# Optimization experiments

Measured on AMD Instinct MI355X. Metric: run time of the kernel, lower is better.

The kernel has to match this reference:

```python
import jax, jax.numpy as jnp
import numpy as np
from jax.scipy.special import gammaln

N_I = 100000
N_J = 100000
D = 8
S_I = 6000
S_J = 6000
NNZ = 500000
EPS = 1e-06


def setup_inputs() -> dict:
    key = jax.random.key(0)
    ks = jax.random.split(key, 9)
    beta = jax.random.normal(ks[0], (N_I,), dtype=jnp.float32)
    gamma = jax.random.normal(ks[1], (N_J,), dtype=jnp.float32)
    latent_zi = jax.random.normal(ks[2], (N_I, D), dtype=jnp.float32)
    latent_zj = jax.random.normal(ks[3], (N_J, D), dtype=jnp.float32)
    # multinomial-without-replacement node samples -> random permutation prefix
    sample_i_idx = jax.random.permutation(ks[4], N_I)[:S_I]
    sample_j_idx = jax.random.permutation(ks[5], N_J)[:S_J]
    # spspmm-selected subgraph links (global node indices) with edge counts
    sparse_i_sample = jax.random.randint(ks[6], (NNZ,), 0, N_I)
    sparse_j_sample = jax.random.randint(ks[7], (NNZ,), 0, N_J)
    valueC = jax.random.uniform(ks[8], (NNZ,), dtype=jnp.float32)
    return {
        'beta': beta, 'gamma': gamma,
        'latent_zi': latent_zi, 'latent_zj': latent_zj,
        'valueC': valueC,
        'sample_i_idx': sample_i_idx, 'sample_j_idx': sample_j_idx,
        'sparse_i_sample': sparse_i_sample, 'sparse_j_sample': sparse_j_sample,
    }


def reference(beta, gamma, latent_zi, latent_zj, valueC,
              sample_i_idx, sample_j_idx, sparse_i_sample, sparse_j_sample):
    # Dense non-link term over sampled (I, J) block
    zi = latent_zi[sample_i_idx]            # [S_I, D]
    zj = latent_zj[sample_j_idx]            # [S_J, D]
    diff = zi[:, None, :] - zj[None, :, :] + EPS   # [S_I, S_J, D]
    z_dist = jnp.sqrt(jnp.sum(diff * diff, axis=-1))  # [S_I, S_J]
    Lambda = beta[sample_i_idx][:, None] + gamma[sample_j_idx][None, :] - z_dist
    # Sparse link terms (Poisson log-likelihood)
    dl = latent_zi[sparse_i_sample] - latent_zj[sparse_j_sample] + EPS  # [NNZ, D]
    z_dist_links = jnp.sqrt(jnp.sum(dl * dl, axis=-1))                  # [NNZ]
    bias_links = beta[sparse_i_sample] + gamma[sparse_j_sample]
    log_Lambda_links = valueC * (bias_links - z_dist_links)
    LL = jnp.sum(log_Lambda_links - gammaln(valueC + 1.0)) - jnp.sum(jnp.exp(Lambda))
    return LL
```

## Files before the change

kernel.cpp:

```cpp
#include <hip/hip_runtime.h>
#include <hip/hip_fp16.h>
#include <math.h>

#define NI_TOT 100000
#define NJ_TOT 100000
#define DD 8
#define SI_N 6000
#define SJ_N 6000
#define NNZ_N 500000
#define EPSF 1e-6f
#define LOG2E 1.44269504088896f

#define TI 64
#define JPT 2
#define JTILE (256 * JPT)
#define ND_I ((SI_N + TI - 1) / TI)
#define NJT ((SJ_N + JTILE - 1) / JTILE)
#define N_DENSE_BLOCKS (ND_I * NJT)
#define LPT 4
#define SPARSE_SPAN (256 * LPT)
#define N_SPARSE_BLOCKS ((NNZ_N + SPARSE_SPAN - 1) / SPARSE_SPAN)
#define N_TOTAL_BLOCKS (N_DENSE_BLOCKS + N_SPARSE_BLOCKS)

#define NROWS (NI_TOT + NJ_TOT)
#define HZ_BYTES ((size_t)NROWS * DD * 2)
#define HB_BYTES ((size_t)NROWS * 2)

#define GA1 (-0.577191652f)
#define GA2 ( 0.988205891f)
#define GA3 (-0.897056937f)
#define GA4 ( 0.918206857f)
#define GA5 (-0.756704078f)
#define GA6 ( 0.482199394f)
#define GA7 (-0.193527818f)
#define GA8 ( 0.035868343f)

__global__ __launch_bounds__(256) void pack_kernel(
    const float* __restrict__ beta, const float* __restrict__ gamma,
    const float* __restrict__ zi_all, const float* __restrict__ zj_all,
    __half* __restrict__ hz, __half* __restrict__ hb)
{
    const int r = blockIdx.x * 256 + threadIdx.x;
    if (r < NROWS) {
        const float* src = (r < NI_TOT) ? zi_all + (size_t)r * DD
                                        : zj_all + (size_t)(r - NI_TOT) * DD;
        float4 a = ((const float4*)src)[0];
        float4 b = ((const float4*)src)[1];
        __half2 h0 = __floats2half2_rn(a.x, a.y);
        __half2 h1 = __floats2half2_rn(a.z, a.w);
        __half2 h2 = __floats2half2_rn(b.x, b.y);
        __half2 h3 = __floats2half2_rn(b.z, b.w);
        uint4 u;
        u.x = *(unsigned*)&h0; u.y = *(unsigned*)&h1;
        u.z = *(unsigned*)&h2; u.w = *(unsigned*)&h3;
        ((uint4*)hz)[r] = u;
    } else if (r < 2 * NROWS) {
        const int q = r - NROWS;
        float v = (q < NI_TOT) ? beta[q] : gamma[q - NI_TOT];
        hb[q] = __float2half(v);
    }
}

__device__ __forceinline__ void unpack_row(uint4 u, float f[DD]) {
    float2 p;
    p = __half22float2(*(__half2*)&u.x); f[0] = p.x; f[1] = p.y;
    p = __half22float2(*(__half2*)&u.y); f[2] = p.x; f[3] = p.y;
    p = __half22float2(*(__half2*)&u.z); f[4] = p.x; f[5] = p.y;
    p = __half22float2(*(__half2*)&u.w); f[6] = p.x; f[7] = p.y;
}

__global__ __launch_bounds__(256) void fused_kernel(
    const float* __restrict__ beta, const float* __restrict__ gamma,
    const float* __restrict__ zi_all, const float* __restrict__ zj_all,
    const float* __restrict__ valueC,
    const int* __restrict__ si, const int* __restrict__ sj,
    const int* __restrict__ spi, const int* __restrict__ spj,
    const __half* __restrict__ hz, const __half* __restrict__ hb,
    float* __restrict__ out, int mode)
{
    __shared__ float sRed[4];
    const int t = threadIdx.x;

    float blocksum = 0.0f;

    if (blockIdx.x < N_DENSE_BLOCKS) {
        __shared__ __align__(16) float  sZi[TI * DD];
        __shared__ __align__(8)  float2 sIB[TI];

        const int it = blockIdx.x % ND_I;
        const int js = blockIdx.x / ND_I;
        const int i0 = it * TI;

        for (int idx = t; idx < TI * DD; idx += 256) {
            int r = idx >> 3, d = idx & 7;
            int gi = i0 + r;
            float v = (gi < SI_N) ? zi_all[(size_t)si[gi] * DD + d] : 0.0f;
            sZi[idx] = (v + EPSF) * LOG2E;
        }
        __syncthreads();
        if (t < TI) {
            int gi = i0 + t;
            float s = 0.0f;
#pragma unroll
            for (int d = 0; d < DD; ++d) {
                float v = sZi[t * DD + d];
                s = fmaf(v, v, s);
            }
            float bL = (gi < SI_N) ? beta[si[gi]] * LOG2E : -1e30f;
            sIB[t] = make_float2(s, bL);
        }

        const int jb = js * JTILE + t * JPT;
        float zA[DD], zB[DD], glA, glB, s2A, s2B;
        {
            int gj = jb;
            if (gj < SJ_N) {
                int row = sj[gj];
                const float4* q = (const float4*)(zj_all + (size_t)row * DD);
                float4 q0 = q[0], q1 = q[1];
                zA[0]=q0.x*LOG2E; zA[1]=q0.y*LOG2E; zA[2]=q0.z*LOG2E; zA[3]=q0.w*LOG2E;
                zA[4]=q1.x*LOG2E; zA[5]=q1.y*LOG2E; zA[6]=q1.z*LOG2E; zA[7]=q1.w*LOG2E;
                glA = gamma[row] * LOG2E;
            } else {
#pragma unroll
                for (int d = 0; d < DD; ++d) zA[d] = 0.0f;
                glA = -1e30f;
            }
            gj = jb + 1;
            if (gj < SJ_N) {
                int row = sj[gj];
                const float4* q = (const float4*)(zj_all + (size_t)row * DD);
                float4 q0 = q[0], q1 = q[1];
                zB[0]=q0.x*LOG2E; zB[1]=q0.y*LOG2E; zB[2]=q0.z*LOG2E; zB[3]=q0.w*LOG2E;
                zB[4]=q1.x*LOG2E; zB[5]=q1.y*LOG2E; zB[6]=q1.z*LOG2E; zB[7]=q1.w*LOG2E;
                glB = gamma[row] * LOG2E;
            } else {
#pragma unroll
                for (int d = 0; d < DD; ++d) zB[d] = 0.0f;
                glB = -1e30f;
            }
            float sa = 0.0f, sb = 0.0f;
#pragma unroll
            for (int d = 0; d < DD; ++d) {
                sa = fmaf(zA[d], zA[d], sa);
                sb = fmaf(zB[d], zB[d], sb);
            }
            s2A = sa; s2B = sb;
        }
        __syncthreads();

        float acc0 = 0.0f, acc1 = 0.0f;
        float4 cr0 = *(const float4*)&sZi[0];
        float4 cr1 = *(const float4*)&sZi[4];
        float2 cib = sIB[0];
#pragma unroll 4
        for (int a = 0; a < TI; ++a) {
            float4 nr0, nr1; float2 nib;
            if (a + 1 < TI) {
                nr0 = *(const float4*)&sZi[(a + 1) * DD];
                nr1 = *(const float4*)&sZi[(a + 1) * DD + 4];
                nib = sIB[a + 1];
            }
            float dA = 0.0f, dB = 0.0f;
            dA = fmaf(cr0.x, zA[0], dA); dB = fmaf(cr0.x, zB[0], dB);
            dA = fmaf(cr0.y, zA[1], dA); dB = fmaf(cr0.y, zB[1], dB);
            dA = fmaf(cr0.z, zA[2], dA); dB = fmaf(cr0.z, zB[2], dB);
            dA = fmaf(cr0.w, zA[3], dA); dB = fmaf(cr0.w, zB[3], dB);
            dA = fmaf(cr1.x, zA[4], dA); dB = fmaf(cr1.x, zB[4], dB);
            dA = fmaf(cr1.y, zA[5], dA); dB = fmaf(cr1.y, zB[5], dB);
            dA = fmaf(cr1.z, zA[6], dA); dB = fmaf(cr1.z, zB[6], dB);
            dA = fmaf(cr1.w, zA[7], dA); dB = fmaf(cr1.w, zB[7], dB);
            float ssA = fmaf(dA, -2.0f, cib.x + s2A);
            float ssB = fmaf(dB, -2.0f, cib.x + s2B);
            ssA = fmaxf(ssA, 1e-20f);
            ssB = fmaxf(ssB, 1e-20f);
            float xA = cib.y + glA - __builtin_amdgcn_sqrtf(ssA);
            float xB = cib.y + glB - __builtin_amdgcn_sqrtf(ssB);
            acc0 += __builtin_amdgcn_exp2f(xA);
            acc1 += __builtin_amdgcn_exp2f(xB);
            cr0 = nr0; cr1 = nr1; cib = nib;
        }
        blocksum = -(acc0 + acc1);
    } else {
        const int base = (blockIdx.x - N_DENSE_BLOCKS) * SPARSE_SPAN + t;
        float val = 0.0f;
        const uint4* hzv = (const uint4*)hz;
#pragma unroll
        for (int u = 0; u < LPT; ++u) {
            const int idx = base + u * 256;
            if (idx >= NNZ_N) continue;
            const int i = spi[idx], j = spj[idx];
            const float c = valueC[idx];
            float dist, bg;
            if (mode == 0) {
                uint4 ui = hzv[i];
                uint4 uj = hzv[NI_TOT + j];
                float fi[DD], fj[DD];
                unpack_row(ui, fi);
                unpack_row(uj, fj);
                float ss = 0.0f;
#pragma unroll
                for (int d = 0; d < DD; ++d) {
                    float df = fi[d] - fj[d] + EPSF;
                    ss = fmaf(df, df, ss);
                }
                ss = fmaxf(ss, 1e-20f);
                dist = __builtin_amdgcn_sqrtf(ss);
                bg = __half2float(hb[i]) + __half2float(hb[NI_TOT + j]);
            } else {
                const float4* zi4 = (const float4*)(zi_all + (size_t)i * DD);
                const float4* zj4 = (const float4*)(zj_all + (size_t)j * DD);
                float4 a0 = zi4[0], a1 = zi4[1];
                float4 b0 = zj4[0], b1 = zj4[1];
                float ss = 0.0f, df;
                df = a0.x-b0.x+EPSF; ss = fmaf(df,df,ss);
                df = a0.y-b0.y+EPSF; ss = fmaf(df,df,ss);
                df = a0.z-b0.z+EPSF; ss = fmaf(df,df,ss);
                df = a0.w-b0.w+EPSF; ss = fmaf(df,df,ss);
                df = a1.x-b1.x+EPSF; ss = fmaf(df,df,ss);
                df = a1.y-b1.y+EPSF; ss = fmaf(df,df,ss);
                df = a1.z-b1.z+EPSF; ss = fmaf(df,df,ss);
                df = a1.w-b1.w+EPSF; ss = fmaf(df,df,ss);
                ss = fmaxf(ss, 1e-20f);
                dist = __builtin_amdgcn_sqrtf(ss);
                bg = beta[i] + gamma[j];
            }
            float g = 1.0f + c*(GA1 + c*(GA2 + c*(GA3 + c*(GA4 + c*(GA5
                          + c*(GA6 + c*(GA7 + c*GA8)))))));
            val += c * (bg - dist) - __builtin_amdgcn_logf(g) * (1.0f / LOG2E);
        }
        blocksum = val;
    }

    float acc = blocksum;
#pragma unroll
    for (int off = 32; off; off >>= 1) acc += __shfl_down(acc, off, 64);
    const int lane = t & 63, w = t >> 6;
    if (lane == 0) sRed[w] = acc;
    __syncthreads();
    if (t == 0) atomicAdd(out, sRed[0] + sRed[1] + sRed[2] + sRed[3]);
}

extern "C" void kernel_launch(void* const* d_in, const int* in_sizes, int n_in,
                              void* d_out, int out_size, void* d_ws, size_t ws_size,
                              hipStream_t stream) {
    const float* beta   = (const float*)d_in[0];
    const float* gamma  = (const float*)d_in[1];
    const float* zi     = (const float*)d_in[2];
    const float* zj     = (const float*)d_in[3];
    const float* valueC = (const float*)d_in[4];
    const int* si   = (const int*)d_in[5];
    const int* sjx  = (const int*)d_in[6];
    const int* spi  = (const int*)d_in[7];
    const int* spj  = (const int*)d_in[8];
    float* out = (float*)d_out;

    const size_t need = HZ_BYTES + HB_BYTES;
    hipMemsetAsync(out, 0, sizeof(float), stream);

    if (ws_size >= need) {
        __half* hz = (__half*)d_ws;
        __half* hb = (__half*)((char*)d_ws + HZ_BYTES);
        const int packb = (2 * NROWS + 255) / 256;
        pack_kernel<<<packb, 256, 0, stream>>>(beta, gamma, zi, zj, hz, hb);
        fused_kernel<<<N_TOTAL_BLOCKS, 256, 0, stream>>>(
            beta, gamma, zi, zj, valueC, si, sjx, spi, spj, hz, hb, out, 0);
    } else {
        fused_kernel<<<N_TOTAL_BLOCKS, 256, 0, stream>>>(
            beta, gamma, zi, zj, valueC, si, sjx, spi, spj,
            (const __half*)zi, (const __half*)zi, out, 1);
    }
}
```

Before: 117.1 us.

## Fold output zeroing into pack kernel and load dense tiles from packed halves

Removes the separate memset launch by having the pack kernel zero the output accumulator. In the default path, the dense tile loaders now read the fp16-packed latent rows and biases instead of gathering fp32 rows, so each i-row is loaded by one thread as a single 16-byte read. The sparse span per block is halved to launch more blocks. This trades more precision loss in the dense term for fewer launches and less gather traffic.

After: 118.3 us. About the same (+1.0%).

```diff
diff --git a/kernel.cpp b/kernel.cpp
--- a/kernel.cpp
+++ b/kernel.cpp
@@ -17,7 +17,7 @@
 #define ND_I ((SI_N + TI - 1) / TI)
 #define NJT ((SJ_N + JTILE - 1) / JTILE)
 #define N_DENSE_BLOCKS (ND_I * NJT)
-#define LPT 4
+#define LPT 2
 #define SPARSE_SPAN (256 * LPT)
 #define N_SPARSE_BLOCKS ((NNZ_N + SPARSE_SPAN - 1) / SPARSE_SPAN)
 #define N_TOTAL_BLOCKS (N_DENSE_BLOCKS + N_SPARSE_BLOCKS)
@@ -38,9 +38,10 @@
 __global__ __launch_bounds__(256) void pack_kernel(
     const float* __restrict__ beta, const float* __restrict__ gamma,
     const float* __restrict__ zi_all, const float* __restrict__ zj_all,
-    __half* __restrict__ hz, __half* __restrict__ hb)
+    __half* __restrict__ hz, __half* __restrict__ hb, float* __restrict__ out)
 {
     const int r = blockIdx.x * 256 + threadIdx.x;
+    if (r == 0) out[0] = 0.0f;
     if (r < NROWS) {
         const float* src = (r < NI_TOT) ? zi_all + (size_t)r * DD
                                         : zj_all + (size_t)(r - NI_TOT) * DD;
@@ -80,6 +81,7 @@
 {
     __shared__ float sRed[4];
     const int t = threadIdx.x;
+    const uint4* hzv = (const uint4*)hz;
 
     float blocksum = 0.0f;
 
@@ -91,23 +93,46 @@
         const int js = blockIdx.x / ND_I;
         const int i0 = it * TI;
 
-        for (int idx = t; idx < TI * DD; idx += 256) {
-            int r = idx >> 3, d = idx & 7;
-            int gi = i0 + r;
-            float v = (gi < SI_N) ? zi_all[(size_t)si[gi] * DD + d] : 0.0f;
-            sZi[idx] = (v + EPSF) * LOG2E;
-        }
-        __syncthreads();
-        if (t < TI) {
-            int gi = i0 + t;
-            float s = 0.0f;
-#pragma unroll
-            for (int d = 0; d < DD; ++d) {
-                float v = sZi[t * DD + d];
-                s = fmaf(v, v, s);
-            }
-            float bL = (gi < SI_N) ? beta[si[gi]] * LOG2E : -1e30f;
-            sIB[t] = make_float2(s, bL);
+        if (mode == 0) {
+            if (t < TI) {
+                int gi = i0 + t;
+                float f[DD];
+                float s = 0.0f, bL = -1e30f;
+                if (gi < SI_N) {
+                    int row = si[gi];
+                    unpack_row(hzv[row], f);
+                    bL = __half2float(hb[row]) * LOG2E;
+                } else {
+#pragma unroll
+                    for (int d = 0; d < DD; ++d) f[d] = 0.0f;
+                }
+#pragma unroll
+                for (int d = 0; d < DD; ++d) {
+                    float v = (f[d] + EPSF) * LOG2E;
+                    sZi[t * DD + d] = v;
+                    s = fmaf(v, v, s);
+                }
+                sIB[t] = make_float2(s, bL);
+            }
+        } else {
+            for (int idx = t; idx < TI * DD; idx += 256) {
+                int r = idx >> 3, d = idx & 7;
+                int gi = i0 + r;
+                float v = (gi < SI_N) ? zi_all[(size_t)si[gi] * DD + d] : 0.0f;
+                sZi[idx] = (v + EPSF) * LOG2E;
+            }
+            __syncthreads();
+            if (t < TI) {
+                int gi = i0 + t;
+                float s = 0.0f;
+#pragma unroll
+                for (int d = 0; d < DD; ++d) {
+                    float v = sZi[t * DD + d];
+                    s = fmaf(v, v, s);
+                }
+                float bL = (gi < SI_N) ? beta[si[gi]] * LOG2E : -1e30f;
+                sIB[t] = make_float2(s, bL);
+            }
         }
 
         const int jb = js * JTILE + t * JPT;
@@ -116,11 +141,19 @@
             int gj = jb;
             if (gj < SJ_N) {
                 int row = sj[gj];
-                const float4* q = (const float4*)(zj_all + (size_t)row * DD);
-                float4 q0 = q[0], q1 = q[1];
-                zA[0]=q0.x*LOG2E; zA[1]=q0.y*LOG2E; zA[2]=q0.z*LOG2E; zA[3]=q0.w*LOG2E;
-                zA[4]=q1.x*LOG2E; zA[5]=q1.y*LOG2E; zA[6]=q1.z*LOG2E; zA[7]=q1.w*LOG2E;
-                glA = gamma[row] * LOG2E;
+                if (mode == 0) {
+                    float f[DD];
+                    unpack_row(hzv[NI_TOT + row], f);
+#pragma unroll
+                    for (int d = 0; d < DD; ++d) zA[d] = f[d] * LOG2E;
+                    glA = __half2float(hb[NI_TOT + row]) * LOG2E;
+                } else {
+                    const float4* q = (const float4*)(zj_all + (size_t)row * DD);
+                    float4 q0 = q[0], q1 = q[1];
+                    zA[0]=q0.x*LOG2E; zA[1]=q0.y*LOG2E; zA[2]=q0.z*LOG2E; zA[3]=q0.w*LOG2E;
+                    zA[4]=q1.x*LOG2E; zA[5]=q1.y*LOG2E; zA[6]=q1.z*LOG2E; zA[7]=q1.w*LOG2E;
+                    glA = gamma[row] * LOG2E;
+                }
             } else {
 #pragma unroll
                 for (int d = 0; d < DD; ++d) zA[d] = 0.0f;
@@ -129,11 +162,19 @@
             gj = jb + 1;
             if (gj < SJ_N) {
                 int row = sj[gj];
-                const float4* q = (const float4*)(zj_all + (size_t)row * DD);
-                float4 q0 = q[0], q1 = q[1];
-                zB[0]=q0.x*LOG2E; zB[1]=q0.y*LOG2E; zB[2]=q0.z*LOG2E; zB[3]=q0.w*LOG2E;
-                zB[4]=q1.x*LOG2E; zB[5]=q1.y*LOG2E; zB[6]=q1.z*LOG2E; zB[7]=q1.w*LOG2E;
-                glB = gamma[row] * LOG2E;
+                if (mode == 0) {
+                    float f[DD];
+                    unpack_row(hzv[NI_TOT + row], f);
+#pragma unroll
+                    for (int d = 0; d < DD; ++d) zB[d] = f[d] * LOG2E;
+                    glB = __half2float(hb[NI_TOT + row]) * LOG2E;
+                } else {
+                    const float4* q = (const float4*)(zj_all + (size_t)row * DD);
+                    float4 q0 = q[0], q1 = q[1];
+                    zB[0]=q0.x*LOG2E; zB[1]=q0.y*LOG2E; zB[2]=q0.z*LOG2E; zB[3]=q0.w*LOG2E;
+                    zB[4]=q1.x*LOG2E; zB[5]=q1.y*LOG2E; zB[6]=q1.z*LOG2E; zB[7]=q1.w*LOG2E;
+                    glB = gamma[row] * LOG2E;
+                }
             } else {
 #pragma unroll
                 for (int d = 0; d < DD; ++d) zB[d] = 0.0f;
@@ -184,7 +225,6 @@
     } else {
         const int base = (blockIdx.x - N_DENSE_BLOCKS) * SPARSE_SPAN + t;
         float val = 0.0f;
-        const uint4* hzv = (const uint4*)hz;
 #pragma unroll
         for (int u = 0; u < LPT; ++u) {
             const int idx = base + u * 256;
@@ -256,16 +296,16 @@
     float* out = (float*)d_out;
 
     const size_t need = HZ_BYTES + HB_BYTES;
-    hipMemsetAsync(out, 0, sizeof(float), stream);
 
     if (ws_size >= need) {
         __half* hz = (__half*)d_ws;
         __half* hb = (__half*)((char*)d_ws + HZ_BYTES);
         const int packb = (2 * NROWS + 255) / 256;
-        pack_kernel<<<packb, 256, 0, stream>>>(beta, gamma, zi, zj, hz, hb);
+        pack_kernel<<<packb, 256, 0, stream>>>(beta, gamma, zi, zj, hz, hb, out);
         fused_kernel<<<N_TOTAL_BLOCKS, 256, 0, stream>>>(
             beta, gamma, zi, zj, valueC, si, sjx, spi, spj, hz, hb, out, 0);
     } else {
+        hipMemsetAsync(out, 0, sizeof(float), stream);
         fused_kernel<<<N_TOTAL_BLOCKS, 256, 0, stream>>>(
             beta, gamma, zi, zj, valueC, si, sjx, spi, spj,
             (const __half*)zi, (const __half*)zi, out, 1);
```
